# Kernel tuning notes

Hardware: AMD Instinct MI355X
Metric: run time of the kernel (lower is better)

## Reference

```python
import jax, jax.numpy as jnp
import numpy as np

B, S, H, NH = 4, 1024, 2048, 16
D = H // NH  # head_dim = 128


def setup_inputs() -> dict:
    key = jax.random.key(0)
    ks = jax.random.split(key, 10)
    # RoPE tables: angle[t, j] = t * 10000^(-2j/D), cos/sin of the complex freqs_cis
    t = jnp.arange(S, dtype=jnp.float32)
    inv_freq = 1.0 / (10000.0 ** (jnp.arange(0, D, 2, dtype=jnp.float32) / D))
    ang = t[:, None] * inv_freq[None, :]  # [S, D//2]
    w = 0.02
    return {
        "hidden_states": jax.random.normal(ks[0], (B, S, H), jnp.float32),
        "freqs_cos": jnp.cos(ang),
        "freqs_sin": jnp.sin(ang),
        "attention_mask": jnp.ones((B, 1, 1, S), jnp.float32),
        "Wq": jax.random.normal(ks[1], (H, H), jnp.float32) * w,
        "bq": jnp.zeros((H,), jnp.float32),
        "Wk": jax.random.normal(ks[2], (H, H), jnp.float32) * w,
        "bk": jnp.zeros((H,), jnp.float32),
        "Wv": jax.random.normal(ks[3], (H, H), jnp.float32) * w,
        "bv": jnp.zeros((H,), jnp.float32),
        "Wo": jax.random.normal(ks[4], (H, H), jnp.float32) * w,
        "bo": jnp.zeros((H,), jnp.float32),
    }


def _rope(x, cos, sin):
    # x: [B, S, NH, D]; cos/sin: [S, D//2]. Complex multiply on (even, odd) pairs.
    x2 = x.reshape(x.shape[:-1] + (D // 2, 2))
    x0, x1 = x2[..., 0], x2[..., 1]
    c = cos[None, :, None, :]
    s = sin[None, :, None, :]
    o0 = x0 * c - x1 * s
    o1 = x0 * s + x1 * c
    return jnp.stack([o0, o1], axis=-1).reshape(x.shape)


def reference(hidden_states, freqs_cos, freqs_sin, attention_mask,
              Wq, bq, Wk, bk, Wv, bv, Wo, bo):
    b, s, _ = hidden_states.shape
    q = (hidden_states @ Wq.T + bq).reshape(b, s, NH, D)
    k = (hidden_states @ Wk.T + bk).reshape(b, s, NH, D)
    v = (hidden_states @ Wv.T + bv).reshape(b, s, NH, D)
    q = _rope(q, freqs_cos, freqs_sin)
    k = _rope(k, freqs_cos, freqs_sin)
    # scores: [b, h, q, k]; original scales by sqrt(embed_dim)=sqrt(hidden_size)
    scores = jnp.einsum('bqhd,bkhd->bhqk', q, k) / jnp.sqrt(jnp.float32(H))
    scores = jnp.where(attention_mask == 0, jnp.float32(-1e9), scores)
    probs = jax.nn.softmax(scores, axis=-1)  # dropout is identity in eval
    ctx = jnp.einsum('bhqk,bkhd->bqhd', probs, v).reshape(b, s, H)
    return ctx @ Wo.T + bo
```

## Files before the change

kernel.cpp:

```cpp
#include <hip/hip_runtime.h>
#include <stdint.h>

#define BATCH 4
#define SEQ   1024
#define NHEAD 16
#define DHEAD 128
#define HDIM  2048
#define GM    4096
#define GN    2048
#define GK    2048

typedef __attribute__((ext_vector_type(8)))  short    short8;
typedef __attribute__((ext_vector_type(4)))  float    f32x4;
typedef __attribute__((ext_vector_type(16))) float    f32x16;
typedef __attribute__((ext_vector_type(4)))  uint32_t u32x4;

__device__ __forceinline__ uint16_t f2bf(float f) {
  uint32_t u = __builtin_bit_cast(uint32_t, f);
  u += 0x7fffu + ((u >> 16) & 1u);
  return (uint16_t)(u >> 16);
}
__device__ __forceinline__ float bf2f(uint16_t h) {
  return __builtin_bit_cast(float, (uint32_t)h << 16);
}
__device__ __forceinline__ uint32_t cvtpk(float lo, float hi) {
  uint32_t r;
  asm("v_cvt_pk_bf16_f32 %0, %1, %2" : "=v"(r) : "v"(lo), "v"(hi));
  return r;
}

__device__ __forceinline__ uint32_t swz128(uint32_t a) { return a ^ (((a >> 7) & 7u) << 4); }
__device__ __forceinline__ uint32_t swz256(uint32_t a) { return a ^ (((a >> 8) & 7u) << 4); }

#define GAS __attribute__((address_space(1)))
#define LAS __attribute__((address_space(3)))
__device__ __forceinline__ void gload_lds16(const void* g, void* l) {
  __builtin_amdgcn_global_load_lds((GAS const void*)g, (LAS void*)l, 16, 0, 0);
}

__global__ void cvt_all_kernel(const float* __restrict__ hs,
                               const float* __restrict__ W0, const float* __restrict__ W1,
                               const float* __restrict__ W2, const float* __restrict__ W3,
                               uint16_t* __restrict__ Xbf, uint16_t* __restrict__ Wb) {
  const int bid = blockIdx.x;
  const float* src; uint16_t* dst;
  if (bid < 4096) {
    src = hs + (size_t)bid * 2048;
    dst = Xbf + (size_t)bid * 2048;
  } else {
    const int m = (bid - 4096) >> 11;
    const int blk = (bid - 4096) & 2047;
    const float* Ws = (m == 0) ? W0 : (m == 1) ? W1 : (m == 2) ? W2 : W3;
    src = Ws + (size_t)blk * 2048;
    dst = Wb + (size_t)m * HDIM * HDIM + (size_t)blk * 2048;
  }
  const float4* p = (const float4*)src + (size_t)threadIdx.x * 2;
  float4 a = p[0], b = p[1];
  uint32_t w0 = f2bf(a.x) | ((uint32_t)f2bf(a.y) << 16);
  uint32_t w1 = f2bf(a.z) | ((uint32_t)f2bf(a.w) << 16);
  uint32_t w2 = f2bf(b.x) | ((uint32_t)f2bf(b.y) << 16);
  uint32_t w3 = f2bf(b.z) | ((uint32_t)f2bf(b.w) << 16);
  int4 r; r.x = (int)w0; r.y = (int)w1; r.z = (int)w2; r.w = (int)w3;
  *(int4*)(dst + (size_t)threadIdx.x * 8) = r;
}

__global__ void rope_kernel(uint16_t* __restrict__ kb,
                            const float* __restrict__ fcos, const float* __restrict__ fsin) {
  uint32_t i = blockIdx.x * 256 + threadIdx.x;
  uint16_t* p = kb + (size_t)i * 8;
  uint32_t e0 = i * 8;
  uint32_t row = e0 >> 11;
  uint32_t col = e0 & 2047;
  uint32_t s = row & (SEQ - 1);
  uint32_t pi = (col & (DHEAD - 1)) >> 1;
  float4 cv = *(const float4*)(fcos + (size_t)s * 64 + pi);
  float4 sv = *(const float4*)(fsin + (size_t)s * 64 + pi);
  int4 raw = *(const int4*)p;
  uint16_t u[8]; *(int4*)u = raw;
  float cc[4] = {cv.x, cv.y, cv.z, cv.w}, ss[4] = {sv.x, sv.y, sv.z, sv.w};
#pragma unroll
  for (int t = 0; t < 4; ++t) {
    float x0 = bf2f(u[2 * t]), x1 = bf2f(u[2 * t + 1]);
    float o0 = x0 * cc[t] - x1 * ss[t];
    float o1 = x0 * ss[t] + x1 * cc[t];
    u[2 * t] = f2bf(o0); u[2 * t + 1] = f2bf(o1);
  }
  *(int4*)p = *(int4*)u;
}

template <int MODE>
__device__ __forceinline__ void gemm_body(const uint16_t* __restrict__ A,
                                          const uint16_t* __restrict__ Bw,
                                          const float* __restrict__ bias,
                                          void* __restrict__ Cout) {
  __shared__ __align__(16) char smA[128 * 128];
  __shared__ __align__(16) char smB[128 * 128];
  const int tid = threadIdx.x, lane = tid & 63, wid = tid >> 6;
  const int c = lane & 15, g = lane >> 4;
  const int row0 = blockIdx.x * 128, col0 = blockIdx.y * 128;
  const int wr = wid >> 1, wc = wid & 1;
  f32x4 acc[4][4] = {};
  const uint32_t oBase = wid * 4096 + lane * 16;

  for (int kk = 0; kk < GK; kk += 64) {
#pragma unroll
    for (int q = 0; q < 4; ++q) {
      uint32_t o = oBase + q * 1024;
      uint32_t r = o >> 7;
      uint32_t cb = (o & 127) ^ ((r & 7u) << 4);
      gload_lds16((const char*)A + ((size_t)(row0 + r) * GK + kk) * 2 + cb,
                  smA + wid * 4096 + q * 1024);
      gload_lds16((const char*)Bw + ((size_t)(col0 + r) * GK + kk) * 2 + cb,
                  smB + wid * 4096 + q * 1024);
    }
    __syncthreads();
    short8 af[4][2], bf[4][2];
#pragma unroll
    for (int m = 0; m < 4; ++m) {
      const uint32_t row = (uint32_t)(wr * 64 + m * 16 + c);
#pragma unroll
      for (int ks = 0; ks < 2; ++ks)
        af[m][ks] = *(const short8*)(smA + row * 128 + (((uint32_t)(ks * 64 + g * 16)) ^ ((row & 7u) << 4)));
    }
#pragma unroll
    for (int n = 0; n < 4; ++n) {
      const uint32_t row = (uint32_t)(wc * 64 + n * 16 + c);
#pragma unroll
      for (int ks = 0; ks < 2; ++ks)
        bf[n][ks] = *(const short8*)(smB + row * 128 + (((uint32_t)(ks * 64 + g * 16)) ^ ((row & 7u) << 4)));
    }
#pragma unroll
    for (int m = 0; m < 4; ++m)
#pragma unroll
      for (int n = 0; n < 4; ++n)
#pragma unroll
        for (int ks = 0; ks < 2; ++ks)
          acc[m][n] = __builtin_amdgcn_mfma_f32_16x16x32_bf16(af[m][ks], bf[n][ks], acc[m][n], 0, 0, 0);
    __syncthreads();
  }

  float bn[4];
#pragma unroll
  for (int n = 0; n < 4; ++n) bn[n] = bias[col0 + wc * 64 + n * 16 + c];
#pragma unroll
  for (int m = 0; m < 4; ++m) {
    const int gr = row0 + wr * 64 + m * 16 + g * 4;
#pragma unroll
    for (int n = 0; n < 4; ++n) {
      const int gc = col0 + wc * 64 + n * 16 + c;
#pragma unroll
      for (int jj = 0; jj < 4; ++jj) {
        float v = acc[m][n][jj] + bn[n];
        if (MODE == 1) ((float*)Cout)[(size_t)(gr + jj) * GN + gc] = v;
        else           ((uint16_t*)Cout)[(size_t)(gr + jj) * GN + gc] = f2bf(v);
      }
    }
  }
}

__global__ __launch_bounds__(256, 2) void gemm_qkv_kernel(
    const uint16_t* __restrict__ X,
    const uint16_t* __restrict__ Wq, const uint16_t* __restrict__ Wk, const uint16_t* __restrict__ Wv,
    const float* __restrict__ bq, const float* __restrict__ bk, const float* __restrict__ bv,
    uint16_t* __restrict__ qo, uint16_t* __restrict__ ko, uint16_t* __restrict__ vo) {
  const uint16_t* W; const float* bias; uint16_t* out;
  if (blockIdx.z == 0)      { W = Wq; bias = bq; out = qo; }
  else if (blockIdx.z == 1) { W = Wk; bias = bk; out = ko; }
  else                      { W = Wv; bias = bv; out = vo; }
  gemm_body<0>(X, W, bias, out);
}

__global__ __launch_bounds__(256, 2) void gemm_out_kernel(
    const uint16_t* __restrict__ ctx, const uint16_t* __restrict__ Wo,
    const float* __restrict__ bo, float* __restrict__ out) {
  gemm_body<1>(ctx, Wo, bo, out);
}

__global__ __launch_bounds__(256, 2) void attn_kernel(
    const uint16_t* __restrict__ q, const uint16_t* __restrict__ k,
    const uint16_t* __restrict__ v, const float* __restrict__ mask,
    const float* __restrict__ fcos, const float* __restrict__ fsin,
    uint16_t* __restrict__ ctx) {
  __shared__ __align__(16) char pool[66048];
  float* smT = (float*)pool;

  const int tid = threadIdx.x, lane = tid & 63, wid = tid >> 6;
  const int c32 = lane & 31, hi = lane >> 5;
  const int lb = (blockIdx.x & 7) * 64 + (blockIdx.x >> 3);
  const int qt = lb & 7, bh = lb >> 3;
  const int h = bh & (NHEAD - 1), b = bh >> 4;
  const int q0 = qt * 128;
  const float scale = 0.022097086912079608f;

  short8 qreg[8];
  {
    const int srow = q0 + wid * 32 + c32;
    const uint16_t* qrow = q + (size_t)(b * SEQ + srow) * HDIM + h * DHEAD;
#pragma unroll
    for (int ks = 0; ks < 8; ++ks) {
      short8 raw = *(const short8*)(qrow + ks * 16 + hi * 8);
      float4 cv = *(const float4*)(fcos + (size_t)srow * 64 + ks * 8 + hi * 4);
      float4 sv = *(const float4*)(fsin + (size_t)srow * 64 + ks * 8 + hi * 4);
      uint16_t u[8]; *(short8*)u = raw;
      float cc[4] = {cv.x, cv.y, cv.z, cv.w}, ssv[4] = {sv.x, sv.y, sv.z, sv.w};
#pragma unroll
      for (int tp = 0; tp < 4; ++tp) {
        float x0 = bf2f(u[2 * tp]), x1 = bf2f(u[2 * tp + 1]);
        u[2 * tp]     = f2bf(x0 * cc[tp] - x1 * ssv[tp]);
        u[2 * tp + 1] = f2bf(x0 * ssv[tp] + x1 * cc[tp]);
      }
      qreg[ks] = *(short8*)u;
    }
  }

  const int kvg = tid >> 5;
  const int d0v = (tid & 31) * 4;

  auto issueK = [&](int s) {
    char* dK = pool + (s & 1) * 16384;
#pragma unroll
    for (int i = 0; i < 4; ++i) {
      uint32_t o_ = wid * 4096 + i * 1024 + lane * 16;
      uint32_t r = o_ >> 8;
      uint32_t cb = swz256(o_) & 255;
      gload_lds16((const char*)k + ((size_t)(b * SEQ + s * 64 + r) * HDIM + h * DHEAD) * 2 + cb,
                  dK + wid * 4096 + i * 1024);
    }
  };
  auto loadV = [&](int s, uint32_t vw[8][2]) {
    const uint16_t* vsrc = v + (size_t)(b * SEQ + s * 64 + kvg * 8) * HDIM + h * DHEAD + d0v;
#pragma unroll
    for (int e = 0; e < 8; ++e) {
      uint2 t2 = *(const uint2*)(vsrc + (size_t)e * HDIM);
      vw[e][0] = t2.x; vw[e][1] = t2.y;
    }
  };
  auto writeVT = [&](int s, uint32_t vw[8][2]) {
    char* dVT = pool + 32768 + (s & 1) * 16384;
#pragma unroll
    for (int j = 0; j < 4; ++j) {
      const int hw = j >> 1, sh = (j & 1) * 16;
      int4 pk;
      pk.x = (int)(((vw[0][hw] >> sh) & 0xffffu) | (((vw[1][hw] >> sh) & 0xffffu) << 16));
      pk.y = (int)(((vw[2][hw] >> sh) & 0xffffu) | (((vw[3][hw] >> sh) & 0xffffu) << 16));
      pk.z = (int)(((vw[4][hw] >> sh) & 0xffffu) | (((vw[5][hw] >> sh) & 0xffffu) << 16));
      pk.w = (int)(((vw[6][hw] >> sh) & 0xffffu) | (((vw[7][hw] >> sh) & 0xffffu) << 16));
      *(int4*)(dVT + swz128((uint32_t)((d0v + j) * 128 + kvg * 16))) = pk;
    }
  };

  float mreg = -1e30f, lreg = 0.f;
  f32x16 o[4] = {};

  {
    float mtmp = 0.f;
    if (tid < 64) mtmp = mask[b * SEQ + tid];
    uint32_t vw[8][2];
    loadV(0, vw);
    issueK(0);
    if (tid < 64) ((float*)(pool + 65536))[tid] = mtmp;
    writeVT(0, vw);
  }
  __syncthreads();

  for (int t = 0; t < 16; ++t) {
    const int cur = t & 1;
    const char* sK  = pool + cur * 16384;
    const char* sVT = pool + 32768 + cur * 16384;
    const float* smMaskF = (const float*)(pool + 65536 + cur * 256);

    float mtmp = 0.f;
    uint32_t vw[8][2];
    if (t < 15) {
      if (tid < 64) mtmp = mask[b * SEQ + (t + 1) * 64 + tid];
      loadV(t + 1, vw);
      issueK(t + 1);
    }

    f32x16 st[2] = {};
    __builtin_amdgcn_s_setprio(1);
#pragma unroll
    for (int ks = 0; ks < 8; ++ks) {
#pragma unroll
      for (int mi = 0; mi < 2; ++mi) {
        const uint32_t row = (uint32_t)(mi * 32 + c32);
        short8 kf = *(const short8*)(sK + row * 256 +
                    (((uint32_t)(ks * 32 + hi * 16)) ^ ((row & 7u) << 4)));
        st[mi] = __builtin_amdgcn_mfma_f32_32x32x16_bf16(kf, qreg[ks], st[mi], 0, 0, 0);
      }
    }
    __builtin_amdgcn_s_setprio(0);

    float p[32];
    float pmax = -1e30f;
#pragma unroll
    for (int mi = 0; mi < 2; ++mi) {
      const float* mb = smMaskF + mi * 32 + hi * 4;
      float4 m0 = *(const float4*)(mb);
      float4 m1 = *(const float4*)(mb + 8);
      float4 m2 = *(const float4*)(mb + 16);
      float4 m3 = *(const float4*)(mb + 24);
      float mm[16] = {m0.x, m0.y, m0.z, m0.w, m1.x, m1.y, m1.z, m1.w,
                      m2.x, m2.y, m2.z, m2.w, m3.x, m3.y, m3.z, m3.w};
#pragma unroll
      for (int r = 0; r < 16; ++r) {
        float s = st[mi][r] * scale;
        if (mm[r] == 0.f) s = -1e9f;
        p[mi * 16 + r] = s;
        pmax = fmaxf(pmax, s);
      }
    }
    pmax = fmaxf(pmax, __shfl_xor(pmax, 32, 64));

    if (!__all(pmax <= mreg + 8.f)) {
      float mnew = fmaxf(mreg, pmax);
      float fac = __expf(mreg - mnew);
      lreg *= fac;
#pragma unroll
      for (int dt = 0; dt < 4; ++dt)
#pragma unroll
        for (int e = 0; e < 16; ++e) o[dt][e] *= fac;
      mreg = mnew;
    }

    float rsum = 0.f;
    short8 pfrag[4];
#pragma unroll
    for (int mi = 0; mi < 2; ++mi) {
      float pe[16];
#pragma unroll
      for (int r = 0; r < 16; ++r) {
        pe[r] = __expf(p[mi * 16 + r] - mreg);
        rsum += pe[r];
      }
      uint32_t w[8], s[8];
#pragma unroll
      for (int j = 0; j < 8; ++j) w[j] = cvtpk(pe[2 * j], pe[2 * j + 1]);
#pragma unroll
      for (int j = 0; j < 8; ++j) s[j] = (uint32_t)__shfl_xor((int)w[j], 32, 64);
      u32x4 f0, f1;
      f0[0] = hi ? s[2] : w[0];  f0[1] = hi ? s[3] : w[1];
      f0[2] = hi ? w[2] : s[0];  f0[3] = hi ? w[3] : s[1];
      f1[0] = hi ? s[6] : w[4];  f1[1] = hi ? s[7] : w[5];
      f1[2] = hi ? w[6] : s[4];  f1[3] = hi ? w[7] : s[5];
      pfrag[mi * 2]     = __builtin_bit_cast(short8, f0);
      pfrag[mi * 2 + 1] = __builtin_bit_cast(short8, f1);
    }
    rsum += __shfl_xor(rsum, 32, 64);
    lreg += rsum;

    if (t < 15) {
      if (tid < 64) ((float*)(pool + 65536 + ((t + 1) & 1) * 256))[tid] = mtmp;
      writeVT(t + 1, vw);
    }

    __builtin_amdgcn_s_setprio(1);
#pragma unroll
    for (int dt = 0; dt < 4; ++dt) {
      const uint32_t row = (uint32_t)(dt * 32 + c32);
#pragma unroll
      for (int e = 0; e < 4; ++e) {
        short8 vf = *(const short8*)(sVT + row * 128 +
                    (((uint32_t)(e * 32 + hi * 16)) ^ ((row & 7u) << 4)));
        o[dt] = __builtin_amdgcn_mfma_f32_32x32x16_bf16(vf, pfrag[e], o[dt], 0, 0, 0);
      }
    }
    __builtin_amdgcn_s_setprio(0);

    __syncthreads();
  }

  const float linv = 1.f / lreg;
  float* myT = smT + wid * (32 * 36);
  const int qe = lane >> 1, de0 = (lane & 1) * 16;
#pragma unroll
  for (int dt = 0; dt < 4; ++dt) {
#pragma unroll
    for (int r = 0; r < 16; ++r) {
      const int drow = (r & 3) + 8 * (r >> 2) + 4 * hi;
      myT[c32 * 36 + drow] = o[dt][r] * linv;
    }
    float vv[16];
#pragma unroll
    for (int j = 0; j < 4; ++j) {
      float4 rd = *(const float4*)(myT + qe * 36 + de0 + j * 4);
      vv[j * 4 + 0] = rd.x; vv[j * 4 + 1] = rd.y; vv[j * 4 + 2] = rd.z; vv[j * 4 + 3] = rd.w;
    }
    uint32_t pw[8];
#pragma unroll
    for (int m = 0; m < 8; ++m)
      pw[m] = f2bf(vv[2 * m]) | ((uint32_t)f2bf(vv[2 * m + 1]) << 16);
    uint16_t* dst = ctx + (size_t)(b * SEQ + q0 + wid * 32 + qe) * HDIM + h * DHEAD + dt * 32 + de0;
    int4 s0; s0.x = (int)pw[0]; s0.y = (int)pw[1]; s0.z = (int)pw[2]; s0.w = (int)pw[3];
    int4 s1; s1.x = (int)pw[4]; s1.y = (int)pw[5]; s1.z = (int)pw[6]; s1.w = (int)pw[7];
    *(int4*)(dst) = s0;
    *(int4*)(dst + 8) = s1;
  }
}

extern "C" void kernel_launch(void* const* d_in, const int* in_sizes, int n_in,
                              void* d_out, int out_size, void* d_ws, size_t ws_size,
                              hipStream_t stream) {
  const float* hs   = (const float*)d_in[0];
  const float* fcos = (const float*)d_in[1];
  const float* fsin = (const float*)d_in[2];
  const float* mask = (const float*)d_in[3];
  const float* Wq = (const float*)d_in[4];  const float* bq = (const float*)d_in[5];
  const float* Wk = (const float*)d_in[6];  const float* bk = (const float*)d_in[7];
  const float* Wv = (const float*)d_in[8];  const float* bv = (const float*)d_in[9];
  const float* Wo = (const float*)d_in[10]; const float* bo = (const float*)d_in[11];
  float* out = (float*)d_out;

  char* ws = (char*)d_ws;
  const size_t XB = (size_t)GM * HDIM * 2;
  const size_t WB = (size_t)HDIM * HDIM * 2;
  uint16_t* Xbf = (uint16_t*)(ws);
  uint16_t* Wqb = (uint16_t*)(ws + XB);
  uint16_t* Wkb = (uint16_t*)(ws + XB + WB);
  uint16_t* Wvb = (uint16_t*)(ws + XB + 2 * WB);
  uint16_t* Wob = (uint16_t*)(ws + XB + 3 * WB);
  uint16_t* qb  = (uint16_t*)(ws + XB + 4 * WB);
  uint16_t* kb  = (uint16_t*)(ws + XB + 4 * WB + XB);
  uint16_t* vb  = (uint16_t*)(ws + XB + 4 * WB + 2 * XB);

  cvt_all_kernel<<<12288, 256, 0, stream>>>(hs, Wq, Wk, Wv, Wo, Xbf, Wqb);

  gemm_qkv_kernel<<<dim3(GM / 128, GN / 128, 3), 256, 0, stream>>>(
      Xbf, Wqb, Wkb, Wvb, bq, bk, bv, qb, kb, vb);

  rope_kernel<<<dim3((GM * HDIM) / 8 / 256, 1, 1), 256, 0, stream>>>(kb, fcos, fsin);

  attn_kernel<<<512, 256, 0, stream>>>(qb, kb, vb, mask, fcos, fsin, Xbf);

  gemm_out_kernel<<<dim3(GM / 128, GN / 128, 1), 256, 0, stream>>>(Xbf, Wob, bo, out);
}
```

Before: 241.0 us.

## Replace QKV GEMM with 256x256-tile 8-wave double-buffered pipelined kernel

The QKV projection GEMM now uses a dedicated kernel with 256x256 output tiles, 512 threads and 128 KB of LDS. A and B are double-buffered, global-to-LDS loads for future k-steps are interleaved between four MFMA quadrant phases, and explicit barriers, waitcnts and setprio control the schedule. The aim is more data reuse per tile and hiding memory latency behind MFMA work. In exchange occupancy drops to one block per CU, and the grid shrinks to 16x8x3 = 384 blocks, which can leave some CUs poorly balanced.

```diff
diff --git a/kernel.cpp b/kernel.cpp
--- a/kernel.cpp
+++ b/kernel.cpp
@@ -9,6 +9,7 @@
 #define GM    4096
 #define GN    2048
 #define GK    2048
+#define NT    32
 
 typedef __attribute__((ext_vector_type(8)))  short    short8;
 typedef __attribute__((ext_vector_type(4)))  float    f32x4;
@@ -37,6 +38,11 @@
 __device__ __forceinline__ void gload_lds16(const void* g, void* l) {
   __builtin_amdgcn_global_load_lds((GAS const void*)g, (LAS void*)l, 16, 0, 0);
 }
+
+#define BARX  __builtin_amdgcn_s_barrier()
+#define LGKM0 do { asm volatile("s_waitcnt lgkmcnt(0)" ::: "memory"); __builtin_amdgcn_sched_barrier(0); } while (0)
+#define VM6   asm volatile("s_waitcnt vmcnt(6)" ::: "memory")
+#define VM0   asm volatile("s_waitcnt vmcnt(0)" ::: "memory")
 
 __global__ void cvt_all_kernel(const float* __restrict__ hs,
                                const float* __restrict__ W0, const float* __restrict__ W1,
@@ -88,11 +94,144 @@
   *(int4*)p = *(int4*)u;
 }
 
-template <int MODE>
-__device__ __forceinline__ void gemm_body(const uint16_t* __restrict__ A,
-                                          const uint16_t* __restrict__ Bw,
-                                          const float* __restrict__ bias,
-                                          void* __restrict__ Cout) {
+__global__ __launch_bounds__(512, 1) void gemm_qkv8_kernel(
+    const uint16_t* __restrict__ A,
+    const uint16_t* __restrict__ W0, const uint16_t* __restrict__ W1, const uint16_t* __restrict__ W2,
+    const float* __restrict__ b0, const float* __restrict__ b1, const float* __restrict__ b2,
+    uint16_t* __restrict__ o0, uint16_t* __restrict__ o1, uint16_t* __restrict__ o2) {
+  __shared__ __align__(16) char ldsA[65536];
+  __shared__ __align__(16) char ldsB[65536];
+  const int tid = threadIdx.x, lane = tid & 63, wid = tid >> 6;
+  const int c = lane & 15, g = lane >> 4;
+  const int wr = wid >> 2, wc = wid & 3;
+  const int row0 = blockIdx.x * 256, col0 = blockIdx.y * 256;
+  const uint16_t* W = (blockIdx.z == 0) ? W0 : (blockIdx.z == 1) ? W1 : W2;
+  const float* bias = (blockIdx.z == 0) ? b0 : (blockIdx.z == 1) ? b1 : b2;
+  uint16_t* outp = (blockIdx.z == 0) ? o0 : (blockIdx.z == 1) ? o1 : o2;
+
+  const uint32_t colswz = ((uint32_t)((lane & 7) ^ (lane >> 3))) << 4;
+  const int srow = wid * 16 + (lane >> 3);
+
+  auto stA = [&](int t, int h) {
+    int ts = (t < NT) ? t : 0;
+    char* d = ldsA + (t & 1) * 32768 + (h * 128 + wid * 16) * 128;
+    const char* s = (const char*)A + ((size_t)(row0 + h * 128 + srow) * GK + (size_t)ts * 64) * 2 + colswz;
+    gload_lds16(s, d);
+    gload_lds16(s + (size_t)8 * GK * 2, d + 1024);
+  };
+  auto stB = [&](int t, int h) {
+    int ts = (t < NT) ? t : 0;
+    char* d = ldsB + (t & 1) * 32768 + (h * 128 + wid * 16) * 128;
+    const char* s = (const char*)W + ((size_t)(col0 + h * 128 + srow) * GK + (size_t)ts * 64) * 2 + colswz;
+    gload_lds16(s, d);
+    gload_lds16(s + (size_t)8 * GK * 2, d + 1024);
+  };
+  auto ldA = [&](int buf, int row, int ks) -> short8 {
+    return *(const short8*)(ldsA + buf * 32768 + row * 128 +
+                            (((uint32_t)(ks * 64 + g * 16)) ^ (((uint32_t)row & 7u) << 4)));
+  };
+  auto ldB = [&](int buf, int row, int ks) -> short8 {
+    return *(const short8*)(ldsB + buf * 32768 + row * 128 +
+                            (((uint32_t)(ks * 64 + g * 16)) ^ (((uint32_t)row & 7u) << 4)));
+  };
+
+  f32x4 acc[8][4] = {};
+
+  stA(0, 0); stA(0, 1); stB(0, 0); stB(0, 1);
+  stA(1, 0); stB(1, 0); stB(1, 1);
+  VM6; BARX;
+
+  short8 af[4][2], bf[2][2], bf2[2][2];
+  for (int t = 0; t < NT; ++t) {
+    const int bufR = t & 1;
+#pragma unroll
+    for (int mi = 0; mi < 4; ++mi)
+#pragma unroll
+      for (int ks = 0; ks < 2; ++ks) af[mi][ks] = ldA(bufR, wr * 128 + mi * 16 + c, ks);
+#pragma unroll
+    for (int nj = 0; nj < 2; ++nj)
+#pragma unroll
+      for (int ks = 0; ks < 2; ++ks) bf[nj][ks] = ldB(bufR, wc * 64 + nj * 16 + c, ks);
+    stA(t + 1, 1);
+    BARX; LGKM0;
+    __builtin_amdgcn_s_setprio(1);
+#pragma unroll
+    for (int mi = 0; mi < 4; ++mi)
+#pragma unroll
+      for (int nj = 0; nj < 2; ++nj)
+#pragma unroll
+        for (int ks = 0; ks < 2; ++ks)
+          acc[mi][nj] = __builtin_amdgcn_mfma_f32_16x16x32_bf16(af[mi][ks], bf[nj][ks], acc[mi][nj], 0, 0, 0);
+    __builtin_amdgcn_s_setprio(0);
+    BARX;
+#pragma unroll
+    for (int nj = 0; nj < 2; ++nj)
+#pragma unroll
+      for (int ks = 0; ks < 2; ++ks) bf2[nj][ks] = ldB(bufR, wc * 64 + (2 + nj) * 16 + c, ks);
+    BARX; LGKM0;
+    __builtin_amdgcn_s_setprio(1);
+#pragma unroll
+    for (int mi = 0; mi < 4; ++mi)
+#pragma unroll
+      for (int nj = 0; nj < 2; ++nj)
+#pragma unroll
+        for (int ks = 0; ks < 2; ++ks)
+          acc[mi][2 + nj] = __builtin_amdgcn_mfma_f32_16x16x32_bf16(af[mi][ks], bf2[nj][ks], acc[mi][2 + nj], 0, 0, 0);
+    __builtin_amdgcn_s_setprio(0);
+    BARX;
+#pragma unroll
+    for (int mi = 0; mi < 4; ++mi)
+#pragma unroll
+      for (int ks = 0; ks < 2; ++ks) af[mi][ks] = ldA(bufR, wr * 128 + (4 + mi) * 16 + c, ks);
+    stB(t + 2, 0);
+    BARX; LGKM0;
+    __builtin_amdgcn_s_setprio(1);
+#pragma unroll
+    for (int mi = 0; mi < 4; ++mi)
+#pragma unroll
+      for (int nj = 0; nj < 2; ++nj)
+#pragma unroll
+        for (int ks = 0; ks < 2; ++ks)
+          acc[4 + mi][nj] = __builtin_amdgcn_mfma_f32_16x16x32_bf16(af[mi][ks], bf[nj][ks], acc[4 + mi][nj], 0, 0, 0);
+    __builtin_amdgcn_s_setprio(0);
+    BARX;
+    stB(t + 2, 1);
+    stA(t + 2, 0);
+    VM6;
+    BARX;
+    __builtin_amdgcn_s_setprio(1);
+#pragma unroll
+    for (int mi = 0; mi < 4; ++mi)
+#pragma unroll
+      for (int nj = 0; nj < 2; ++nj)
+#pragma unroll
+        for (int ks = 0; ks < 2; ++ks)
+          acc[4 + mi][2 + nj] = __builtin_amdgcn_mfma_f32_16x16x32_bf16(af[mi][ks], bf2[nj][ks], acc[4 + mi][2 + nj], 0, 0, 0);
+    __builtin_amdgcn_s_setprio(0);
+    BARX;
+  }
+  VM0;
+
+  float bn[4];
+#pragma unroll
+  for (int nj = 0; nj < 4; ++nj) bn[nj] = bias[col0 + wc * 64 + nj * 16 + c];
+#pragma unroll
+  for (int mi = 0; mi < 8; ++mi) {
+#pragma unroll
+    for (int jj = 0; jj < 4; ++jj) {
+      const int row = row0 + wr * 128 + mi * 16 + g * 4 + jj;
+#pragma unroll
+      for (int nj = 0; nj < 4; ++nj) {
+        const int d = wc * 64 + nj * 16 + c;
+        outp[(size_t)row * GN + col0 + d] = f2bf(acc[mi][nj][jj] + bn[nj]);
+      }
+    }
+  }
+}
+
+__global__ __launch_bounds__(256, 2) void gemm_out_kernel(
+    const uint16_t* __restrict__ A, const uint16_t* __restrict__ Bw,
+    const float* __restrict__ bias, float* __restrict__ Cout) {
   __shared__ __align__(16) char smA[128 * 128];
   __shared__ __align__(16) char smB[128 * 128];
   const int tid = threadIdx.x, lane = tid & 63, wid = tid >> 6;
@@ -149,31 +288,10 @@
     for (int n = 0; n < 4; ++n) {
       const int gc = col0 + wc * 64 + n * 16 + c;
 #pragma unroll
-      for (int jj = 0; jj < 4; ++jj) {
-        float v = acc[m][n][jj] + bn[n];
-        if (MODE == 1) ((float*)Cout)[(size_t)(gr + jj) * GN + gc] = v;
-        else           ((uint16_t*)Cout)[(size_t)(gr + jj) * GN + gc] = f2bf(v);
-      }
-    }
-  }
-}
-
-__global__ __launch_bounds__(256, 2) void gemm_qkv_kernel(
-    const uint16_t* __restrict__ X,
-    const uint16_t* __restrict__ Wq, const uint16_t* __restrict__ Wk, const uint16_t* __restrict__ Wv,
-    const float* __restrict__ bq, const float* __restrict__ bk, const float* __restrict__ bv,
-    uint16_t* __restrict__ qo, uint16_t* __restrict__ ko, uint16_t* __restrict__ vo) {
-  const uint16_t* W; const float* bias; uint16_t* out;
-  if (blockIdx.z == 0)      { W = Wq; bias = bq; out = qo; }
-  else if (blockIdx.z == 1) { W = Wk; bias = bk; out = ko; }
-  else                      { W = Wv; bias = bv; out = vo; }
-  gemm_body<0>(X, W, bias, out);
-}
-
-__global__ __launch_bounds__(256, 2) void gemm_out_kernel(
-    const uint16_t* __restrict__ ctx, const uint16_t* __restrict__ Wo,
-    const float* __restrict__ bo, float* __restrict__ out) {
-  gemm_body<1>(ctx, Wo, bo, out);
+      for (int jj = 0; jj < 4; ++jj)
+        Cout[(size_t)(gr + jj) * GN + gc] = acc[m][n][jj] + bn[n];
+    }
+  }
 }
 
 __global__ __launch_bounds__(256, 2) void attn_kernel(
@@ -425,7 +543,7 @@
 
   cvt_all_kernel<<<12288, 256, 0, stream>>>(hs, Wq, Wk, Wv, Wo, Xbf, Wqb);
 
-  gemm_qkv_kernel<<<dim3(GM / 128, GN / 128, 3), 256, 0, stream>>>(
+  gemm_qkv8_kernel<<<dim3(GM / 256, GN / 256, 3), 512, 0, stream>>>(
       Xbf, Wqb, Wkb, Wvb, bq, bk, bv, qb, kb, vb);
 
   rope_kernel<<<dim3((GM * HDIM) / 8 / 256, 1, 1), 256, 0, stream>>>(kb, fcos, fsin);
```

Measured after the change: 264.3 us. 1.1x slower.
